# Kernel tuning notes

Hardware: AMD Instinct MI355X
Metric: run time of the kernel (lower is better)

## Reference

```python
import jax, jax.numpy as jnp
import numpy as np

N, T, H, O, S, R = 64, 1024, 256, 80, 128, 2


def _lin(k, fin, fout):
    kw, kb = jax.random.split(k)
    s = 1.0 / np.sqrt(fin)
    return (jax.random.uniform(kw, (fout, fin), jnp.float32, -s, s),
            jax.random.uniform(kb, (fout,), jnp.float32, -s, s))


def _gru_params(k, fin, hid):
    k1, k2, k3, k4 = jax.random.split(k, 4)
    s = 1.0 / np.sqrt(hid)
    u = lambda kk, shp: jax.random.uniform(kk, shp, jnp.float32, -s, s)
    return u(k1, (3 * hid, fin)), u(k2, (3 * hid, hid)), u(k3, (3 * hid,)), u(k4, (3 * hid,))


def setup_inputs() -> dict:
    key = jax.random.key(0)
    ks = jax.random.split(key, 16)
    inp = {}
    inp["input_enc"] = jax.random.normal(ks[0], (N, T, 2 * H), jnp.float32)
    inp["input_attW_enc"] = jax.random.normal(ks[1], (N, T, 2 * H), jnp.float32)
    inp["input_dec"] = jax.random.normal(ks[2], (N, O), jnp.float32)
    inp["style_vec"] = jax.random.normal(ks[3], (N, 1, S), jnp.float32)
    lengths = jnp.sort(jax.random.randint(ks[4], (N,), 1, T + 1))[::-1]
    inp["lengths_enc"] = lengths.at[0].set(T)  # pack_padded requires max(len)==T, descending
    inp["pw1"], inp["pb1"] = _lin(ks[5], O, 2 * H)
    inp["pw2"], inp["pb2"] = _lin(ks[6], 2 * H, H)
    inp["wdec"], inp["bdec"] = _lin(ks[7], 2 * H, 2 * H)
    inp["ga_ih"], inp["ga_hh"], inp["ga_bih"], inp["ga_bhh"] = _gru_params(ks[8], 3 * H + S, 2 * H)
    inp["wattn"], inp["battn"] = _lin(ks[9], 2 * H, 1)
    inp["wsc"], inp["bsc"] = _lin(ks[10], 4 * H + S, 2 * H)
    inp["g1_ih"], inp["g1_hh"], inp["g1_bih"], inp["g1_bhh"] = _gru_params(ks[11], 4 * H + S, 2 * H)
    inp["g2_ih"], inp["g2_hh"], inp["g2_bih"], inp["g2_bhh"] = _gru_params(ks[12], 2 * H, 2 * H)
    inp["wout"], inp["bout"] = _lin(ks[13], 2 * H, R * O)
    return inp


def _gru_cell(x, h, w_ih, w_hh, b_ih, b_hh):
    # PyTorch GRU cell: gates order (r, z, n)
    gi = x @ w_ih.T + b_ih
    gh = h @ w_hh.T + b_hh
    ir, iz, inn = jnp.split(gi, 3, -1)
    hr, hz, hn = jnp.split(gh, 3, -1)
    r = jax.nn.sigmoid(ir + hr)
    z = jax.nn.sigmoid(iz + hz)
    n = jnp.tanh(inn + r * hn)
    return (1.0 - z) * n + z * h


def reference(input_enc, input_attW_enc, input_dec, style_vec,
              pw1, pb1, pw2, pb2, wdec, bdec,
              ga_ih, ga_hh, ga_bih, ga_bhh,
              wattn, battn, wsc, bsc,
              g1_ih, g1_hh, g1_bih, g1_bhh,
              g2_ih, g2_hh, g2_bih, g2_bhh,
              wout, bout, lengths_enc):
    Nn, Tt, D2 = input_enc.shape
    Hh = D2 // 2
    # prenet (dropout disabled: eval-mode reference)
    pre = jax.nn.relu(jax.nn.relu(input_dec @ pw1.T + pb1) @ pw2.T + pb2)  # (N,H)
    ctx0 = jnp.zeros((Nn, 2 * Hh), input_enc.dtype)  # input_context=None -> zeros
    sv = style_vec[:, 0, :]
    x_att = jnp.concatenate([pre, ctx0, sv], axis=-1)  # (N,3H+S)
    h0 = jnp.zeros((Nn, 2 * Hh), input_enc.dtype)  # hidden states start None -> zeros
    out_att = _gru_cell(x_att, h0, ga_ih, ga_hh, ga_bih, ga_bhh)  # (N,2H)
    attW_dec = out_att @ wdec.T + bdec  # (N,2H), broadcast over T (expand_as)
    e = jnp.tanh(input_attW_enc + attW_dec[:, None, :])  # (N,T,2H)
    score = e @ wattn.T + battn  # (N,T,1)
    mask = (jnp.arange(Tt)[None, :] < lengths_enc[:, None]).astype(score.dtype)[..., None]
    w = jnp.exp(score) * mask  # pack/pad zeroes padded positions
    w = w / jnp.maximum(jnp.sum(w, axis=1, keepdims=True), 1e-12)  # F.normalize(p=1, dim=1)
    attn_applied = jnp.einsum('nt,ntd->nd', w[..., 0], input_enc)  # bmm(w^T, enc) -> (N,2H)
    out_dec = jnp.concatenate([attn_applied, out_att, sv], axis=-1)  # (N,4H+S)
    residual = out_dec @ wsc.T + bsc
    h1 = _gru_cell(out_dec, h0, g1_ih, g1_hh, g1_bih, g1_bhh)
    residual = residual + h1
    h2 = _gru_cell(residual, h0, g2_ih, g2_hh, g2_bih, g2_bhh)
    residual = residual + h2
    output = (residual @ wout.T + bout).reshape(Nn, R, -1)  # (N,r,O)
    return output, attn_applied[:, None, :]
```

## Files before the change

kernel.cpp:

```cpp
#include <hip/hip_runtime.h>
#include <math.h>

#define NB  64
#define TT  1024
#define H2  512
#define SS  128
#define OO  80
#define FIN_A 896
#define FIN_1 1152
#define CH  32

__device__ __forceinline__ float fast_rcp(float x) { return __builtin_amdgcn_rcpf(x); }
__device__ __forceinline__ float fast_sigmoid(float x) { return fast_rcp(1.0f + __expf(-x)); }
__device__ __forceinline__ float fast_tanh(float x) {
    float e = __expf(2.0f * x);
    return 1.0f - 2.0f * fast_rcp(e + 1.0f);
}
__device__ __forceinline__ float wred(float p) {
    #pragma unroll
    for (int o = 32; o > 0; o >>= 1) p += __shfl_xor(p, o, 64);
    return p;
}

__global__ void k_l1(const float* __restrict__ xdec, const float* __restrict__ pw1,
                     const float* __restrict__ pb1, const float* __restrict__ sv,
                     float* __restrict__ t1T, float* __restrict__ xaT,
                     float* __restrict__ out_decT) {
    int wv = threadIdx.x >> 6, lane = threadIdx.x & 63;
    if (blockIdx.x < 128) {
        int i = blockIdx.x * 4 + wv;
        const float* w = pw1 + i * OO;
        const float* x = xdec + lane * OO;
        float acc = 0.0f;
        #pragma unroll 8
        for (int k = 0; k < OO; ++k) acc += w[k] * x[k];
        t1T[i * 64 + lane] = fmaxf(acc + pb1[i], 0.0f);
    } else {
        int s = (blockIdx.x - 128) * 4 + wv;
        float v = sv[lane * SS + s];
        xaT[(256 + s) * 64 + lane] = v;
        out_decT[(1024 + s) * 64 + lane] = v;
    }
}

__global__ __launch_bounds__(512) void k_l2(const float* __restrict__ t1T,
                                            const float* __restrict__ pw2,
                                            const float* __restrict__ pb2,
                                            float* __restrict__ xaT) {
    int i = blockIdx.x;
    int wv = threadIdx.x >> 6, lane = threadIdx.x & 63;
    int k0 = wv * 64;
    const float* w = pw2 + (size_t)i * H2 + k0;
    const float* xT = t1T + k0 * 64;
    float p = 0.0f;
    #pragma unroll 8
    for (int k = 0; k < 64; ++k) p += w[k] * xT[k * 64 + lane];
    __shared__ float s[8][64];
    s[wv][lane] = p;
    __syncthreads();
    if (wv == 0) {
        float acc = 0.0f;
        #pragma unroll
        for (int q = 0; q < 8; ++q) acc += s[q][lane];
        xaT[i * 64 + lane] = fmaxf(acc + pb2[i], 0.0f);
    }
}

__global__ __launch_bounds__(512) void k_gruA(const float* __restrict__ xaT,
                                              const float* __restrict__ ga_ih,
                                              const float* __restrict__ ga_bih,
                                              const float* __restrict__ ga_bhh,
                                              float* __restrict__ out_decT) {
    int j = blockIdx.x;
    int wv = threadIdx.x >> 6, lane = threadIdx.x & 63;
    int k0 = wv * 48;
    const float* wr = ga_ih + (size_t)j * FIN_A;
    const float* wz = ga_ih + (size_t)(H2 + j) * FIN_A;
    const float* wn = ga_ih + (size_t)(2 * H2 + j) * FIN_A;
    float pr = 0.0f, pz = 0.0f, pn = 0.0f;
    #pragma unroll 8
    for (int kk = 0; kk < 48; ++kk) {
        int k = k0 + kk;
        int wc = k + (k >= 256 ? 512 : 0);
        float xv = xaT[k * 64 + lane];
        pr += wr[wc] * xv; pz += wz[wc] * xv; pn += wn[wc] * xv;
    }
    __shared__ float s[3][8][64];
    s[0][wv][lane] = pr; s[1][wv][lane] = pz; s[2][wv][lane] = pn;
    __syncthreads();
    if (wv == 0) {
        float fr = 0.0f, fz = 0.0f, fn = 0.0f;
        #pragma unroll
        for (int q = 0; q < 8; ++q) { fr += s[0][q][lane]; fz += s[1][q][lane]; fn += s[2][q][lane]; }
        float r = fast_sigmoid(fr + ga_bih[j] + ga_bhh[j]);
        float z = fast_sigmoid(fz + ga_bih[H2 + j] + ga_bhh[H2 + j]);
        float nn = fast_tanh(fn + ga_bih[2 * H2 + j] + r * ga_bhh[2 * H2 + j]);
        out_decT[(H2 + j) * 64 + lane] = (1.0f - z) * nn;
    }
}

__global__ __launch_bounds__(512) void k_attw(const float* __restrict__ out_decT,
                                              const float* __restrict__ wdec,
                                              const float* __restrict__ bdec,
                                              float* __restrict__ attW_dec) {
    int i = blockIdx.x;
    int wv = threadIdx.x >> 6, lane = threadIdx.x & 63;
    int k0 = wv * 64;
    const float* w = wdec + (size_t)i * H2 + k0;
    const float* xT = out_decT + (H2 + k0) * 64;
    float p = 0.0f;
    #pragma unroll 8
    for (int k = 0; k < 64; ++k) p += w[k] * xT[k * 64 + lane];
    __shared__ float s[8][64];
    s[wv][lane] = p;
    __syncthreads();
    if (wv == 0) {
        float acc = 0.0f;
        #pragma unroll
        for (int q = 0; q < 8; ++q) acc += s[q][lane];
        attW_dec[lane * H2 + i] = acc + bdec[i];
    }
}

__global__ __launch_bounds__(256) void k_attn(
        const float* __restrict__ enc, const float* __restrict__ attw_enc,
        const float* __restrict__ attW_dec, const float* __restrict__ wattn,
        const float* __restrict__ battn, const int* __restrict__ lengths,
        float* __restrict__ num_part ,
        float* __restrict__ den_part ) {
    int p = blockIdx.y;
    int c = blockIdx.x;
    int wv = threadIdx.x >> 6, lane = threadIdx.x & 63;
    int t0 = c * (TT / CH);
    __shared__ float sew[TT / CH];
    __shared__ float s[4 * 512];
    __shared__ float sd[4];
    const float4* w4 = (const float4*)wattn;
    float b = battn[0];

    #pragma unroll
    for (int half = 0; half < 2; ++half) {
        int n = half ? (63 - p) : p;
        int len = lengths[n];

        {
            const float4* d4 = (const float4*)(attW_dec + n * H2);
            #pragma unroll
            for (int r = 0; r < 8; ++r) {
                int t = t0 + wv * 8 + r;
                float val = 0.0f;
                if (t < len) {
                    const float4* e4 = (const float4*)(attw_enc + ((size_t)(n * TT + t)) * H2);
                    float pp = 0.0f;
                    #pragma unroll
                    for (int m = 0; m < 2; ++m) {
                        int idx = lane + m * 64;
                        float4 e = e4[idx], d = d4[idx], w = w4[idx];
                        pp += fast_tanh(e.x + d.x) * w.x + fast_tanh(e.y + d.y) * w.y +
                              fast_tanh(e.z + d.z) * w.z + fast_tanh(e.w + d.w) * w.w;
                    }
                    pp = wred(pp);
                    val = __expf(pp + b);
                }
                if (lane == 0) sew[wv * 8 + r] = val;
            }
        }
        __syncthreads();

        int d0 = lane * 8;
        const float* base = enc + ((size_t)(n * TT + t0 + wv * 8)) * H2 + d0;
        float4 a0 = {0, 0, 0, 0}, a1 = {0, 0, 0, 0};
        float dp = 0.0f;
        #pragma unroll
        for (int r = 0; r < 8; ++r) {
            float wt = sew[wv * 8 + r];
            if (wt != 0.0f) {
                const float4* v4 = (const float4*)(base + (size_t)r * H2);
                float4 v0 = v4[0], v1 = v4[1];
                a0.x += wt * v0.x; a0.y += wt * v0.y; a0.z += wt * v0.z; a0.w += wt * v0.w;
                a1.x += wt * v1.x; a1.y += wt * v1.y; a1.z += wt * v1.z; a1.w += wt * v1.w;
                dp += wt;
            }
        }
        float4* srow = (float4*)(s + wv * 512 + d0);
        srow[0] = a0; srow[1] = a1;
        if (lane == 0) sd[wv] = dp;
        __syncthreads();
        int d = threadIdx.x;
        float r0 = s[d] + s[512 + d] + s[1024 + d] + s[1536 + d];
        float r1 = s[256 + d] + s[768 + d] + s[1280 + d] + s[1792 + d];
        float* np = num_part + ((size_t)(c * NB + n)) * H2;
        np[d] = r0;
        np[256 + d] = r1;
        if (threadIdx.x == 0) den_part[c * NB + n] = sd[0] + sd[1] + sd[2] + sd[3];
        __syncthreads();
    }
}

__global__ void k_reduce(const float* __restrict__ num_part, const float* __restrict__ den_part,
                         float* __restrict__ out, float* __restrict__ out_decT) {
    int n = blockIdx.x;
    int d = blockIdx.y * 256 + threadIdx.x;
    float s = 0.0f, den = 0.0f;
    #pragma unroll 8
    for (int c = 0; c < CH; ++c) {
        s += num_part[((size_t)(c * NB + n)) * H2 + d];
        den += den_part[c * NB + n];
    }
    float a = s / fmaxf(den, 1e-12f);
    out[NB * 160 + n * H2 + d] = a;
    out_decT[(size_t)d * 64 + n] = a;
}

__global__ __launch_bounds__(512) void k_sc_h1(const float* __restrict__ out_decT,
                                               const float* __restrict__ wsc,
                                               const float* __restrict__ bsc,
                                               const float* __restrict__ g1_ih,
                                               const float* __restrict__ g1_bih,
                                               const float* __restrict__ g1_bhh,
                                               float* __restrict__ res1T) {
    int j = blockIdx.x;
    int wv = threadIdx.x >> 6, lane = threadIdx.x & 63;
    int k0 = wv * 144;
    const float* ws_ = wsc + (size_t)j * FIN_1 + k0;
    const float* wr = g1_ih + (size_t)j * FIN_1 + k0;
    const float* wz = g1_ih + (size_t)(H2 + j) * FIN_1 + k0;
    const float* wn = g1_ih + (size_t)(2 * H2 + j) * FIN_1 + k0;
    const float* xT = out_decT + k0 * 64;
    float2 ps = {0, 0}, pr = {0, 0}, pz = {0, 0}, pn = {0, 0};
    #pragma unroll 4
    for (int k = 0; k < 144; k += 2) {
        float x0 = xT[k * 64 + lane];
        float x1 = xT[(k + 1) * 64 + lane];
        float2 a = *(const float2*)(ws_ + k);
        float2 bb = *(const float2*)(wr + k);
        float2 cc = *(const float2*)(wz + k);
        float2 dd = *(const float2*)(wn + k);
        ps.x += a.x * x0; ps.y += a.y * x1;
        pr.x += bb.x * x0; pr.y += bb.y * x1;
        pz.x += cc.x * x0; pz.y += cc.y * x1;
        pn.x += dd.x * x0; pn.y += dd.y * x1;
    }
    __shared__ float s[4][8][64];
    s[0][wv][lane] = ps.x + ps.y; s[1][wv][lane] = pr.x + pr.y;
    s[2][wv][lane] = pz.x + pz.y; s[3][wv][lane] = pn.x + pn.y;
    __syncthreads();
    if (wv == 0) {
        float fs = 0.0f, fr = 0.0f, fz = 0.0f, fn = 0.0f;
        #pragma unroll
        for (int q = 0; q < 8; ++q) {
            fs += s[0][q][lane]; fr += s[1][q][lane];
            fz += s[2][q][lane]; fn += s[3][q][lane];
        }
        float r = fast_sigmoid(fr + g1_bih[j] + g1_bhh[j]);
        float z = fast_sigmoid(fz + g1_bih[H2 + j] + g1_bhh[H2 + j]);
        float nn = fast_tanh(fn + g1_bih[2 * H2 + j] + r * g1_bhh[2 * H2 + j]);
        res1T[j * 64 + lane] = fs + bsc[j] + (1.0f - z) * nn;
    }
}

__global__ __launch_bounds__(512) void k_h2(const float* __restrict__ res1T,
                                            const float* __restrict__ g2_ih,
                                            const float* __restrict__ g2_bih,
                                            const float* __restrict__ g2_bhh,
                                            float* __restrict__ res2T) {
    int j = blockIdx.x;
    int wv = threadIdx.x >> 6, lane = threadIdx.x & 63;
    int k0 = wv * 64;
    const float* wr = g2_ih + (size_t)j * H2 + k0;
    const float* wz = g2_ih + (size_t)(H2 + j) * H2 + k0;
    const float* wn = g2_ih + (size_t)(2 * H2 + j) * H2 + k0;
    const float* xT = res1T + k0 * 64;
    float pr = 0.0f, pz = 0.0f, pn = 0.0f;
    #pragma unroll 8
    for (int k = 0; k < 64; ++k) {
        float xv = xT[k * 64 + lane];
        pr += wr[k] * xv; pz += wz[k] * xv; pn += wn[k] * xv;
    }
    __shared__ float s[3][8][64];
    s[0][wv][lane] = pr; s[1][wv][lane] = pz; s[2][wv][lane] = pn;
    __syncthreads();
    if (wv == 0) {
        float fr = 0.0f, fz = 0.0f, fn = 0.0f;
        #pragma unroll
        for (int q = 0; q < 8; ++q) { fr += s[0][q][lane]; fz += s[1][q][lane]; fn += s[2][q][lane]; }
        float r = fast_sigmoid(fr + g2_bih[j] + g2_bhh[j]);
        float z = fast_sigmoid(fz + g2_bih[H2 + j] + g2_bhh[H2 + j]);
        float nn = fast_tanh(fn + g2_bih[2 * H2 + j] + r * g2_bhh[2 * H2 + j]);
        res2T[j * 64 + lane] = res1T[j * 64 + lane] + (1.0f - z) * nn;
    }
}

__global__ __launch_bounds__(512) void k_out(const float* __restrict__ res2T,
                                             const float* __restrict__ wout,
                                             const float* __restrict__ bout,
                                             float* __restrict__ out) {
    int i = blockIdx.x;
    int wv = threadIdx.x >> 6, lane = threadIdx.x & 63;
    int k0 = wv * 64;
    const float* w = wout + (size_t)i * H2 + k0;
    const float* xT = res2T + k0 * 64;
    float p = 0.0f;
    #pragma unroll 8
    for (int k = 0; k < 64; ++k) p += w[k] * xT[k * 64 + lane];
    __shared__ float s[8][64];
    s[wv][lane] = p;
    __syncthreads();
    if (wv == 0) {
        float acc = 0.0f;
        #pragma unroll
        for (int q = 0; q < 8; ++q) acc += s[q][lane];
        out[lane * 160 + i] = acc + bout[i];
    }
}

extern "C" void kernel_launch(void* const* d_in, const int* in_sizes, int n_in,
                              void* d_out, int out_size, void* d_ws, size_t ws_size,
                              hipStream_t stream) {
    const float* input_enc      = (const float*)d_in[0];
    const float* input_attW_enc = (const float*)d_in[1];
    const float* input_dec      = (const float*)d_in[2];
    const float* style_vec      = (const float*)d_in[3];
    const int*   lengths_enc    = (const int*)d_in[4];
    const float* pw1  = (const float*)d_in[5];
    const float* pb1  = (const float*)d_in[6];
    const float* pw2  = (const float*)d_in[7];
    const float* pb2  = (const float*)d_in[8];
    const float* wdec = (const float*)d_in[9];
    const float* bdec = (const float*)d_in[10];
    const float* ga_ih  = (const float*)d_in[11];
    const float* ga_bih = (const float*)d_in[13];
    const float* ga_bhh = (const float*)d_in[14];
    const float* wattn  = (const float*)d_in[15];
    const float* battn  = (const float*)d_in[16];
    const float* wsc    = (const float*)d_in[17];
    const float* bsc    = (const float*)d_in[18];
    const float* g1_ih  = (const float*)d_in[19];
    const float* g1_bih = (const float*)d_in[21];
    const float* g1_bhh = (const float*)d_in[22];
    const float* g2_ih  = (const float*)d_in[23];
    const float* g2_bih = (const float*)d_in[25];
    const float* g2_bhh = (const float*)d_in[26];
    const float* wout   = (const float*)d_in[27];
    const float* bout   = (const float*)d_in[28];
    float* out = (float*)d_out;

    float* ws = (float*)d_ws;
    float* num_part = ws;
    float* den_part = ws + 1048576;
    float* t1T      = ws + 1050624;
    float* xaT      = ws + 1083392;
    float* out_decT = ws + 1107968;
    float* attW_dec = ws + 1181696;
    float* res1T    = ws + 1214464;
    float* res2T    = ws + 1247232;

    k_l1<<<160, 256, 0, stream>>>(input_dec, pw1, pb1, style_vec, t1T, xaT, out_decT);
    k_l2<<<256, 512, 0, stream>>>(t1T, pw2, pb2, xaT);
    k_gruA<<<512, 512, 0, stream>>>(xaT, ga_ih, ga_bih, ga_bhh, out_decT);
    k_attw<<<512, 512, 0, stream>>>(out_decT, wdec, bdec, attW_dec);
    k_attn<<<dim3(CH, 32), 256, 0, stream>>>(input_enc, input_attW_enc, attW_dec,
                                             wattn, battn, lengths_enc, num_part, den_part);
    k_reduce<<<dim3(64, 2), 256, 0, stream>>>(num_part, den_part, out, out_decT);
    k_sc_h1<<<512, 512, 0, stream>>>(out_decT, wsc, bsc, g1_ih, g1_bih, g1_bhh, res1T);
    k_h2<<<512, 512, 0, stream>>>(res1T, g2_ih, g2_bih, g2_bhh, res2T);
    k_out<<<160, 512, 0, stream>>>(res2T, wout, bout, out);
}
```

Measured before the change: 383.3 us.

## Fuse all stages into one cooperative persistent kernel with grid syncs

Replaces the nine separate kernel launches with a single cooperative kernel of 1024 blocks that runs every stage in sequence, separated by grid-wide barriers. Stages keep the prior per-block work mapping, with 256-thread blocks replacing the earlier 512-thread ones for the GEMV stages. The aim is to remove launch gaps and per-kernel tail effects. In exchange it adds eight grid.sync barriers and leaves many blocks idle in the small stages. It falls back to the old multi-kernel path if cooperative launch or the required occupancy is unavailable.

```diff
diff --git a/kernel.cpp b/kernel.cpp
--- a/kernel.cpp
+++ b/kernel.cpp
@@ -1,5 +1,8 @@
 #include <hip/hip_runtime.h>
+#include <hip/hip_cooperative_groups.h>
 #include <math.h>
+
+namespace cg = cooperative_groups;
 
 #define NB  64
 #define TT  1024
@@ -20,6 +23,289 @@
     #pragma unroll
     for (int o = 32; o > 0; o >>= 1) p += __shfl_xor(p, o, 64);
     return p;
+}
+
+__global__ __launch_bounds__(256, 4) void mega(
+        const float* __restrict__ enc, const float* __restrict__ attw_enc,
+        const float* __restrict__ xdec, const float* __restrict__ sv,
+        const int* __restrict__ lengths,
+        const float* __restrict__ pw1, const float* __restrict__ pb1,
+        const float* __restrict__ pw2, const float* __restrict__ pb2,
+        const float* __restrict__ wdec, const float* __restrict__ bdec,
+        const float* __restrict__ ga_ih, const float* __restrict__ ga_bih,
+        const float* __restrict__ ga_bhh,
+        const float* __restrict__ wattn, const float* __restrict__ battn,
+        const float* __restrict__ wsc, const float* __restrict__ bsc,
+        const float* __restrict__ g1_ih, const float* __restrict__ g1_bih,
+        const float* __restrict__ g1_bhh,
+        const float* __restrict__ g2_ih, const float* __restrict__ g2_bih,
+        const float* __restrict__ g2_bhh,
+        const float* __restrict__ wout, const float* __restrict__ bout,
+        float* __restrict__ out,
+        float* __restrict__ num_part, float* __restrict__ den_part,
+        float* __restrict__ t1T, float* __restrict__ xaT,
+        float* __restrict__ out_decT, float* __restrict__ attW_dec,
+        float* __restrict__ res1T, float* __restrict__ res2T) {
+    cg::grid_group grid = cg::this_grid();
+    int b = blockIdx.x;
+    int wv = threadIdx.x >> 6, lane = threadIdx.x & 63;
+    __shared__ float smem[2112];
+
+    if (b < 128) {
+        int i = b * 4 + wv;
+        const float* w = pw1 + i * OO;
+        const float* x = xdec + lane * OO;
+        float acc = 0.0f;
+        #pragma unroll 8
+        for (int k = 0; k < OO; ++k) acc += w[k] * x[k];
+        t1T[i * 64 + lane] = fmaxf(acc + pb1[i], 0.0f);
+    } else if (b < 160) {
+        int s = (b - 128) * 4 + wv;
+        float v = sv[lane * SS + s];
+        xaT[(256 + s) * 64 + lane] = v;
+        out_decT[(1024 + s) * 64 + lane] = v;
+    }
+    grid.sync();
+
+    if (b < 256) {
+        int i = b, k0 = wv * 128;
+        const float* w = pw2 + (size_t)i * H2 + k0;
+        const float* xT = t1T + k0 * 64;
+        float p = 0.0f;
+        #pragma unroll 8
+        for (int k = 0; k < 128; ++k) p += w[k] * xT[k * 64 + lane];
+        smem[wv * 64 + lane] = p;
+        __syncthreads();
+        if (wv == 0) {
+            float acc = smem[lane] + smem[64 + lane] + smem[128 + lane] + smem[192 + lane];
+            xaT[i * 64 + lane] = fmaxf(acc + pb2[i], 0.0f);
+        }
+    }
+    grid.sync();
+
+    if (b < 512) {
+        int j = b, k0 = wv * 96;
+        const float* wr = ga_ih + (size_t)j * FIN_A;
+        const float* wz = ga_ih + (size_t)(H2 + j) * FIN_A;
+        const float* wn = ga_ih + (size_t)(2 * H2 + j) * FIN_A;
+        float pr = 0.0f, pz = 0.0f, pn = 0.0f;
+        #pragma unroll 8
+        for (int kk = 0; kk < 96; ++kk) {
+            int k = k0 + kk;
+            int wc = k + (k >= 256 ? 512 : 0);
+            float xv = xaT[k * 64 + lane];
+            pr += wr[wc] * xv; pz += wz[wc] * xv; pn += wn[wc] * xv;
+        }
+        smem[wv * 64 + lane] = pr;
+        smem[256 + wv * 64 + lane] = pz;
+        smem[512 + wv * 64 + lane] = pn;
+        __syncthreads();
+        if (wv == 0) {
+            float fr = 0.0f, fz = 0.0f, fn = 0.0f;
+            #pragma unroll
+            for (int q = 0; q < 4; ++q) {
+                fr += smem[q * 64 + lane];
+                fz += smem[256 + q * 64 + lane];
+                fn += smem[512 + q * 64 + lane];
+            }
+            float r = fast_sigmoid(fr + ga_bih[j] + ga_bhh[j]);
+            float z = fast_sigmoid(fz + ga_bih[H2 + j] + ga_bhh[H2 + j]);
+            float nn = fast_tanh(fn + ga_bih[2 * H2 + j] + r * ga_bhh[2 * H2 + j]);
+            out_decT[(H2 + j) * 64 + lane] = (1.0f - z) * nn;
+        }
+    }
+    grid.sync();
+
+    if (b < 512) {
+        int i = b, k0 = wv * 128;
+        const float* w = wdec + (size_t)i * H2 + k0;
+        const float* xT = out_decT + (H2 + k0) * 64;
+        float p = 0.0f;
+        #pragma unroll 8
+        for (int k = 0; k < 128; ++k) p += w[k] * xT[k * 64 + lane];
+        __syncthreads();
+        smem[wv * 64 + lane] = p;
+        __syncthreads();
+        if (wv == 0) {
+            float acc = smem[lane] + smem[64 + lane] + smem[128 + lane] + smem[192 + lane];
+            attW_dec[lane * H2 + i] = acc + bdec[i];
+        }
+    }
+    grid.sync();
+
+    {
+        int c = b & 31, p = b >> 5;
+        int t0 = c * (TT / CH);
+        float* sew = smem;
+        float* sd = smem + 32;
+        float* s = smem + 64;
+        const float4* w4 = (const float4*)wattn;
+        float bb = battn[0];
+        #pragma unroll
+        for (int half = 0; half < 2; ++half) {
+            int n = half ? (63 - p) : p;
+            int len = lengths[n];
+            {
+                const float4* d4 = (const float4*)(attW_dec + n * H2);
+                #pragma unroll
+                for (int r = 0; r < 8; ++r) {
+                    int t = t0 + wv * 8 + r;
+                    float val = 0.0f;
+                    if (t < len) {
+                        const float4* e4 = (const float4*)(attw_enc + ((size_t)(n * TT + t)) * H2);
+                        float pp = 0.0f;
+                        #pragma unroll
+                        for (int m = 0; m < 2; ++m) {
+                            int idx = lane + m * 64;
+                            float4 e = e4[idx], d = d4[idx], w = w4[idx];
+                            pp += fast_tanh(e.x + d.x) * w.x + fast_tanh(e.y + d.y) * w.y +
+                                  fast_tanh(e.z + d.z) * w.z + fast_tanh(e.w + d.w) * w.w;
+                        }
+                        pp = wred(pp);
+                        val = __expf(pp + bb);
+                    }
+                    if (lane == 0) sew[wv * 8 + r] = val;
+                }
+            }
+            __syncthreads();
+            int d0 = lane * 8;
+            const float* base = enc + ((size_t)(n * TT + t0 + wv * 8)) * H2 + d0;
+            float4 a0 = {0, 0, 0, 0}, a1 = {0, 0, 0, 0};
+            float dp = 0.0f;
+            #pragma unroll
+            for (int r = 0; r < 8; ++r) {
+                float wt = sew[wv * 8 + r];
+                if (wt != 0.0f) {
+                    const float4* v4 = (const float4*)(base + (size_t)r * H2);
+                    float4 v0 = v4[0], v1 = v4[1];
+                    a0.x += wt * v0.x; a0.y += wt * v0.y; a0.z += wt * v0.z; a0.w += wt * v0.w;
+                    a1.x += wt * v1.x; a1.y += wt * v1.y; a1.z += wt * v1.z; a1.w += wt * v1.w;
+                    dp += wt;
+                }
+            }
+            float4* srow = (float4*)(s + wv * 512 + d0);
+            srow[0] = a0; srow[1] = a1;
+            if (lane == 0) sd[wv] = dp;
+            __syncthreads();
+            int d = threadIdx.x;
+            float r0 = s[d] + s[512 + d] + s[1024 + d] + s[1536 + d];
+            float r1 = s[256 + d] + s[768 + d] + s[1280 + d] + s[1792 + d];
+            float* np = num_part + ((size_t)(c * NB + n)) * H2;
+            np[d] = r0;
+            np[256 + d] = r1;
+            if (threadIdx.x == 0) den_part[c * NB + n] = sd[0] + sd[1] + sd[2] + sd[3];
+            __syncthreads();
+        }
+    }
+    grid.sync();
+
+    if (b < 128) {
+        int n = b >> 1;
+        int d = (b & 1) * 256 + threadIdx.x;
+        float s = 0.0f, den = 0.0f;
+        #pragma unroll 8
+        for (int c = 0; c < CH; ++c) {
+            s += num_part[((size_t)(c * NB + n)) * H2 + d];
+            den += den_part[c * NB + n];
+        }
+        float a = s / fmaxf(den, 1e-12f);
+        out[NB * 160 + n * H2 + d] = a;
+        out_decT[(size_t)d * 64 + n] = a;
+    }
+    grid.sync();
+
+    if (b < 512) {
+        int j = b, k0 = wv * 288;
+        const float* ws_ = wsc + (size_t)j * FIN_1 + k0;
+        const float* wr = g1_ih + (size_t)j * FIN_1 + k0;
+        const float* wz = g1_ih + (size_t)(H2 + j) * FIN_1 + k0;
+        const float* wn = g1_ih + (size_t)(2 * H2 + j) * FIN_1 + k0;
+        const float* xT = out_decT + k0 * 64;
+        float2 ps = {0, 0}, pr = {0, 0}, pz = {0, 0}, pn = {0, 0};
+        #pragma unroll 4
+        for (int k = 0; k < 288; k += 2) {
+            float x0 = xT[k * 64 + lane];
+            float x1 = xT[(k + 1) * 64 + lane];
+            float2 a = *(const float2*)(ws_ + k);
+            float2 bb2 = *(const float2*)(wr + k);
+            float2 cc = *(const float2*)(wz + k);
+            float2 dd = *(const float2*)(wn + k);
+            ps.x += a.x * x0; ps.y += a.y * x1;
+            pr.x += bb2.x * x0; pr.y += bb2.y * x1;
+            pz.x += cc.x * x0; pz.y += cc.y * x1;
+            pn.x += dd.x * x0; pn.y += dd.y * x1;
+        }
+        __syncthreads();
+        smem[wv * 64 + lane] = ps.x + ps.y;
+        smem[256 + wv * 64 + lane] = pr.x + pr.y;
+        smem[512 + wv * 64 + lane] = pz.x + pz.y;
+        smem[768 + wv * 64 + lane] = pn.x + pn.y;
+        __syncthreads();
+        if (wv == 0) {
+            float fs = 0.0f, fr = 0.0f, fz = 0.0f, fn = 0.0f;
+            #pragma unroll
+            for (int q = 0; q < 4; ++q) {
+                fs += smem[q * 64 + lane];
+                fr += smem[256 + q * 64 + lane];
+                fz += smem[512 + q * 64 + lane];
+                fn += smem[768 + q * 64 + lane];
+            }
+            float r = fast_sigmoid(fr + g1_bih[j] + g1_bhh[j]);
+            float z = fast_sigmoid(fz + g1_bih[H2 + j] + g1_bhh[H2 + j]);
+            float nn = fast_tanh(fn + g1_bih[2 * H2 + j] + r * g1_bhh[2 * H2 + j]);
+            res1T[j * 64 + lane] = fs + bsc[j] + (1.0f - z) * nn;
+        }
+    }
+    grid.sync();
+
+    if (b < 512) {
+        int j = b, k0 = wv * 128;
+        const float* wr = g2_ih + (size_t)j * H2 + k0;
+        const float* wz = g2_ih + (size_t)(H2 + j) * H2 + k0;
+        const float* wn = g2_ih + (size_t)(2 * H2 + j) * H2 + k0;
+        const float* xT = res1T + k0 * 64;
+        float pr = 0.0f, pz = 0.0f, pn = 0.0f;
+        #pragma unroll 8
+        for (int k = 0; k < 128; ++k) {
+            float xv = xT[k * 64 + lane];
+            pr += wr[k] * xv; pz += wz[k] * xv; pn += wn[k] * xv;
+        }
+        __syncthreads();
+        smem[wv * 64 + lane] = pr;
+        smem[256 + wv * 64 + lane] = pz;
+        smem[512 + wv * 64 + lane] = pn;
+        __syncthreads();
+        if (wv == 0) {
+            float fr = 0.0f, fz = 0.0f, fn = 0.0f;
+            #pragma unroll
+            for (int q = 0; q < 4; ++q) {
+                fr += smem[q * 64 + lane];
+                fz += smem[256 + q * 64 + lane];
+                fn += smem[512 + q * 64 + lane];
+            }
+            float r = fast_sigmoid(fr + g2_bih[j] + g2_bhh[j]);
+            float z = fast_sigmoid(fz + g2_bih[H2 + j] + g2_bhh[H2 + j]);
+            float nn = fast_tanh(fn + g2_bih[2 * H2 + j] + r * g2_bhh[2 * H2 + j]);
+            res2T[j * 64 + lane] = res1T[j * 64 + lane] + (1.0f - z) * nn;
+        }
+    }
+    grid.sync();
+
+    if (b < 160) {
+        int i = b, k0 = wv * 128;
+        const float* w = wout + (size_t)i * H2 + k0;
+        const float* xT = res2T + k0 * 64;
+        float p = 0.0f;
+        #pragma unroll 8
+        for (int k = 0; k < 128; ++k) p += w[k] * xT[k * 64 + lane];
+        __syncthreads();
+        smem[wv * 64 + lane] = p;
+        __syncthreads();
+        if (wv == 0) {
+            float acc = smem[lane] + smem[64 + lane] + smem[128 + lane] + smem[192 + lane];
+            out[lane * 160 + i] = acc + bout[i];
+        }
+    }
 }
 
 __global__ void k_l1(const float* __restrict__ xdec, const float* __restrict__ pw1,
@@ -126,8 +412,7 @@
         const float* __restrict__ enc, const float* __restrict__ attw_enc,
         const float* __restrict__ attW_dec, const float* __restrict__ wattn,
         const float* __restrict__ battn, const int* __restrict__ lengths,
-        float* __restrict__ num_part ,
-        float* __restrict__ den_part ) {
+        float* __restrict__ num_part, float* __restrict__ den_part) {
     int p = blockIdx.y;
     int c = blockIdx.x;
     int wv = threadIdx.x >> 6, lane = threadIdx.x & 63;
@@ -142,7 +427,6 @@
     for (int half = 0; half < 2; ++half) {
         int n = half ? (63 - p) : p;
         int len = lengths[n];
-
         {
             const float4* d4 = (const float4*)(attW_dec + n * H2);
             #pragma unroll
@@ -166,7 +450,6 @@
             }
         }
         __syncthreads();
-
         int d0 = lane * 8;
         const float* base = enc + ((size_t)(n * TT + t0 + wv * 8)) * H2 + d0;
         float4 a0 = {0, 0, 0, 0}, a1 = {0, 0, 0, 0};
@@ -355,14 +638,42 @@
     float* res1T    = ws + 1214464;
     float* res2T    = ws + 1247232;
 
-    k_l1<<<160, 256, 0, stream>>>(input_dec, pw1, pb1, style_vec, t1T, xaT, out_decT);
-    k_l2<<<256, 512, 0, stream>>>(t1T, pw2, pb2, xaT);
-    k_gruA<<<512, 512, 0, stream>>>(xaT, ga_ih, ga_bih, ga_bhh, out_decT);
-    k_attw<<<512, 512, 0, stream>>>(out_decT, wdec, bdec, attW_dec);
-    k_attn<<<dim3(CH, 32), 256, 0, stream>>>(input_enc, input_attW_enc, attW_dec,
-                                             wattn, battn, lengths_enc, num_part, den_part);
-    k_reduce<<<dim3(64, 2), 256, 0, stream>>>(num_part, den_part, out, out_decT);
-    k_sc_h1<<<512, 512, 0, stream>>>(out_decT, wsc, bsc, g1_ih, g1_bih, g1_bhh, res1T);
-    k_h2<<<512, 512, 0, stream>>>(res1T, g2_ih, g2_bih, g2_bhh, res2T);
-    k_out<<<160, 512, 0, stream>>>(res2T, wout, bout, out);
-}
+    bool coop_ok = false;
+    int maxBlocksPerCU = 0;
+    if (hipOccupancyMaxActiveBlocksPerMultiprocessor(&maxBlocksPerCU, (const void*)mega,
+                                                     256, 0) == hipSuccess &&
+        maxBlocksPerCU >= 4) {
+        void* args[] = {
+            (void*)&input_enc, (void*)&input_attW_enc, (void*)&input_dec, (void*)&style_vec,
+            (void*)&lengths_enc,
+            (void*)&pw1, (void*)&pb1, (void*)&pw2, (void*)&pb2,
+            (void*)&wdec, (void*)&bdec,
+            (void*)&ga_ih, (void*)&ga_bih, (void*)&ga_bhh,
+            (void*)&wattn, (void*)&battn,
+            (void*)&wsc, (void*)&bsc,
+            (void*)&g1_ih, (void*)&g1_bih, (void*)&g1_bhh,
+            (void*)&g2_ih, (void*)&g2_bih, (void*)&g2_bhh,
+            (void*)&wout, (void*)&bout,
+            (void*)&out,
+            (void*)&num_part, (void*)&den_part, (void*)&t1T, (void*)&xaT,
+            (void*)&out_decT, (void*)&attW_dec, (void*)&res1T, (void*)&res2T
+        };
+        if (hipLaunchCooperativeKernel((const void*)mega, dim3(1024), dim3(256),
+                                       args, 0, stream) == hipSuccess) {
+            coop_ok = true;
+        }
+    }
+
+    if (!coop_ok) {
+        k_l1<<<160, 256, 0, stream>>>(input_dec, pw1, pb1, style_vec, t1T, xaT, out_decT);
+        k_l2<<<256, 512, 0, stream>>>(t1T, pw2, pb2, xaT);
+        k_gruA<<<512, 512, 0, stream>>>(xaT, ga_ih, ga_bih, ga_bhh, out_decT);
+        k_attw<<<512, 512, 0, stream>>>(out_decT, wdec, bdec, attW_dec);
+        k_attn<<<dim3(CH, 32), 256, 0, stream>>>(input_enc, input_attW_enc, attW_dec,
+                                                 wattn, battn, lengths_enc, num_part, den_part);
+        k_reduce<<<dim3(64, 2), 256, 0, stream>>>(num_part, den_part, out, out_decT);
+        k_sc_h1<<<512, 512, 0, stream>>>(out_decT, wsc, bsc, g1_ih, g1_bih, g1_bhh, res1T);
+        k_h2<<<512, 512, 0, stream>>>(res1T, g2_ih, g2_bih, g2_bhh, res2T);
+        k_out<<<160, 512, 0, stream>>>(res2T, wout, bout, out);
+    }
+}
```

Result: no change. 390.0 us (+1.7%).

## Fuse decoder prenet, attention GRU and attW projection into one per-batch kernel

Applied to the files above, without the earlier changes.

Replaces four kernels (prenet layer 1, layer 2, attention GRU, decoder attention projection) with a single kernel that runs one 1024-thread block per batch row and keeps intermediates in shared memory. This removes three launches, their global-memory round trips and the gaps between kernels. In exchange, each of the 64 blocks re-reads all the weight matrices (about 7 MB in total), so weight traffic goes up 64-fold, mostly served from L2. Only 64 blocks run, so most of the GPU's CUs sit idle.

```diff
diff --git a/kernel.cpp b/kernel.cpp
--- a/kernel.cpp
+++ b/kernel.cpp
@@ -22,103 +22,89 @@
     return p;
 }
 
-__global__ void k_l1(const float* __restrict__ xdec, const float* __restrict__ pw1,
-                     const float* __restrict__ pb1, const float* __restrict__ sv,
-                     float* __restrict__ t1T, float* __restrict__ xaT,
-                     float* __restrict__ out_decT) {
-    int wv = threadIdx.x >> 6, lane = threadIdx.x & 63;
-    if (blockIdx.x < 128) {
-        int i = blockIdx.x * 4 + wv;
+__global__ __launch_bounds__(1024) void k_dec(
+        const float* __restrict__ xdec, const float* __restrict__ sv,
+        const float* __restrict__ pw1, const float* __restrict__ pb1,
+        const float* __restrict__ pw2, const float* __restrict__ pb2,
+        const float* __restrict__ ga_ih, const float* __restrict__ ga_bih,
+        const float* __restrict__ ga_bhh,
+        const float* __restrict__ wdec, const float* __restrict__ bdec,
+        float* __restrict__ out_decT, float* __restrict__ attW_dec) {
+    int n = blockIdx.x;
+    int wv = threadIdx.x >> 6, lane = threadIdx.x & 63;
+    __shared__ float st1[512];
+    __shared__ float spre[256];
+    __shared__ float ssv[128];
+    __shared__ float satt[512];
+
+    if (threadIdx.x < 128) {
+        float v = sv[n * SS + threadIdx.x];
+        ssv[threadIdx.x] = v;
+        out_decT[(1024 + threadIdx.x) * 64 + n] = v;
+    }
+
+    const float* x0 = xdec + n * OO;
+    float xa = (lane < OO) ? x0[lane] : 0.0f;
+    float xb = (lane < OO - 64) ? x0[64 + lane] : 0.0f;
+    for (int o = 0; o < 32; ++o) {
+        int i = wv * 32 + o;
         const float* w = pw1 + i * OO;
-        const float* x = xdec + lane * OO;
-        float acc = 0.0f;
-        #pragma unroll 8
-        for (int k = 0; k < OO; ++k) acc += w[k] * x[k];
-        t1T[i * 64 + lane] = fmaxf(acc + pb1[i], 0.0f);
-    } else {
-        int s = (blockIdx.x - 128) * 4 + wv;
-        float v = sv[lane * SS + s];
-        xaT[(256 + s) * 64 + lane] = v;
-        out_decT[(1024 + s) * 64 + lane] = v;
-    }
-}
-
-__global__ __launch_bounds__(512) void k_l2(const float* __restrict__ t1T,
-                                            const float* __restrict__ pw2,
-                                            const float* __restrict__ pb2,
-                                            float* __restrict__ xaT) {
-    int i = blockIdx.x;
-    int wv = threadIdx.x >> 6, lane = threadIdx.x & 63;
-    int k0 = wv * 64;
-    const float* w = pw2 + (size_t)i * H2 + k0;
-    const float* xT = t1T + k0 * 64;
-    float p = 0.0f;
-    #pragma unroll 8
-    for (int k = 0; k < 64; ++k) p += w[k] * xT[k * 64 + lane];
-    __shared__ float s[8][64];
-    s[wv][lane] = p;
-    __syncthreads();
-    if (wv == 0) {
-        float acc = 0.0f;
-        #pragma unroll
-        for (int q = 0; q < 8; ++q) acc += s[q][lane];
-        xaT[i * 64 + lane] = fmaxf(acc + pb2[i], 0.0f);
-    }
-}
-
-__global__ __launch_bounds__(512) void k_gruA(const float* __restrict__ xaT,
-                                              const float* __restrict__ ga_ih,
-                                              const float* __restrict__ ga_bih,
-                                              const float* __restrict__ ga_bhh,
-                                              float* __restrict__ out_decT) {
-    int j = blockIdx.x;
-    int wv = threadIdx.x >> 6, lane = threadIdx.x & 63;
-    int k0 = wv * 48;
-    const float* wr = ga_ih + (size_t)j * FIN_A;
-    const float* wz = ga_ih + (size_t)(H2 + j) * FIN_A;
-    const float* wn = ga_ih + (size_t)(2 * H2 + j) * FIN_A;
-    float pr = 0.0f, pz = 0.0f, pn = 0.0f;
-    #pragma unroll 8
-    for (int kk = 0; kk < 48; ++kk) {
-        int k = k0 + kk;
-        int wc = k + (k >= 256 ? 512 : 0);
-        float xv = xaT[k * 64 + lane];
-        pr += wr[wc] * xv; pz += wz[wc] * xv; pn += wn[wc] * xv;
-    }
-    __shared__ float s[3][8][64];
-    s[0][wv][lane] = pr; s[1][wv][lane] = pz; s[2][wv][lane] = pn;
-    __syncthreads();
-    if (wv == 0) {
-        float fr = 0.0f, fz = 0.0f, fn = 0.0f;
-        #pragma unroll
-        for (int q = 0; q < 8; ++q) { fr += s[0][q][lane]; fz += s[1][q][lane]; fn += s[2][q][lane]; }
-        float r = fast_sigmoid(fr + ga_bih[j] + ga_bhh[j]);
-        float z = fast_sigmoid(fz + ga_bih[H2 + j] + ga_bhh[H2 + j]);
-        float nn = fast_tanh(fn + ga_bih[2 * H2 + j] + r * ga_bhh[2 * H2 + j]);
-        out_decT[(H2 + j) * 64 + lane] = (1.0f - z) * nn;
-    }
-}
-
-__global__ __launch_bounds__(512) void k_attw(const float* __restrict__ out_decT,
-                                              const float* __restrict__ wdec,
-                                              const float* __restrict__ bdec,
-                                              float* __restrict__ attW_dec) {
-    int i = blockIdx.x;
-    int wv = threadIdx.x >> 6, lane = threadIdx.x & 63;
-    int k0 = wv * 64;
-    const float* w = wdec + (size_t)i * H2 + k0;
-    const float* xT = out_decT + (H2 + k0) * 64;
-    float p = 0.0f;
-    #pragma unroll 8
-    for (int k = 0; k < 64; ++k) p += w[k] * xT[k * 64 + lane];
-    __shared__ float s[8][64];
-    s[wv][lane] = p;
-    __syncthreads();
-    if (wv == 0) {
-        float acc = 0.0f;
-        #pragma unroll
-        for (int q = 0; q < 8; ++q) acc += s[q][lane];
-        attW_dec[lane * H2 + i] = acc + bdec[i];
+        float wa = (lane < OO) ? w[lane] : 0.0f;
+        float wb = (lane < OO - 64) ? w[64 + lane] : 0.0f;
+        float p = wred(xa * wa + xb * wb);
+        if (lane == 0) st1[i] = fmaxf(p + pb1[i], 0.0f);
+    }
+    __syncthreads();
+
+    for (int o = 0; o < 16; ++o) {
+        int i = wv * 16 + o;
+        const float* w = pw2 + (size_t)i * H2;
+        float p = 0.0f;
+        #pragma unroll
+        for (int m = 0; m < 8; ++m) { int k = lane + 64 * m; p += w[k] * st1[k]; }
+        p = wred(p);
+        if (lane == 0) spre[i] = fmaxf(p + pb2[i], 0.0f);
+    }
+    __syncthreads();
+
+    for (int o = 0; o < 32; ++o) {
+        int j = wv * 32 + o;
+        const float* wr = ga_ih + (size_t)j * FIN_A;
+        const float* wz = ga_ih + (size_t)(H2 + j) * FIN_A;
+        const float* wn = ga_ih + (size_t)(2 * H2 + j) * FIN_A;
+        float pr = 0.0f, pz = 0.0f, pn = 0.0f;
+        #pragma unroll
+        for (int m = 0; m < 4; ++m) {
+            int k = lane + 64 * m;
+            float xv = spre[k];
+            pr += wr[k] * xv; pz += wz[k] * xv; pn += wn[k] * xv;
+        }
+        #pragma unroll
+        for (int m = 0; m < 2; ++m) {
+            int k = lane + 64 * m;
+            float xv = ssv[k];
+            pr += wr[768 + k] * xv; pz += wz[768 + k] * xv; pn += wn[768 + k] * xv;
+        }
+        pr = wred(pr); pz = wred(pz); pn = wred(pn);
+        if (lane == 0) {
+            float r = fast_sigmoid(pr + ga_bih[j] + ga_bhh[j]);
+            float z = fast_sigmoid(pz + ga_bih[H2 + j] + ga_bhh[H2 + j]);
+            float nn = fast_tanh(pn + ga_bih[2 * H2 + j] + r * ga_bhh[2 * H2 + j]);
+            float oa = (1.0f - z) * nn;
+            satt[j] = oa;
+            out_decT[(H2 + j) * 64 + n] = oa;
+        }
+    }
+    __syncthreads();
+
+    for (int o = 0; o < 32; ++o) {
+        int i = wv * 32 + o;
+        const float* w = wdec + (size_t)i * H2;
+        float p = 0.0f;
+        #pragma unroll
+        for (int m = 0; m < 8; ++m) { int k = lane + 64 * m; p += w[k] * satt[k]; }
+        p = wred(p);
+        if (lane == 0) attW_dec[n * H2 + i] = p + bdec[i];
     }
 }
 
@@ -142,7 +128,6 @@
     for (int half = 0; half < 2; ++half) {
         int n = half ? (63 - p) : p;
         int len = lengths[n];
-
         {
             const float4* d4 = (const float4*)(attW_dec + n * H2);
             #pragma unroll
@@ -166,7 +151,6 @@
             }
         }
         __syncthreads();
-
         int d0 = lane * 8;
         const float* base = enc + ((size_t)(n * TT + t0 + wv * 8)) * H2 + d0;
         float4 a0 = {0, 0, 0, 0}, a1 = {0, 0, 0, 0};
@@ -348,17 +332,14 @@
     float* ws = (float*)d_ws;
     float* num_part = ws;
     float* den_part = ws + 1048576;
-    float* t1T      = ws + 1050624;
-    float* xaT      = ws + 1083392;
-    float* out_decT = ws + 1107968;
-    float* attW_dec = ws + 1181696;
-    float* res1T    = ws + 1214464;
-    float* res2T    = ws + 1247232;
-
-    k_l1<<<160, 256, 0, stream>>>(input_dec, pw1, pb1, style_vec, t1T, xaT, out_decT);
-    k_l2<<<256, 512, 0, stream>>>(t1T, pw2, pb2, xaT);
-    k_gruA<<<512, 512, 0, stream>>>(xaT, ga_ih, ga_bih, ga_bhh, out_decT);
-    k_attw<<<512, 512, 0, stream>>>(out_decT, wdec, bdec, attW_dec);
+    float* out_decT = ws + 1050624;
+    float* attW_dec = ws + 1124352;
+    float* res1T    = ws + 1157120;
+    float* res2T    = ws + 1189888;
+
+    k_dec<<<64, 1024, 0, stream>>>(input_dec, style_vec, pw1, pb1, pw2, pb2,
+                                   ga_ih, ga_bih, ga_bhh, wdec, bdec,
+                                   out_decT, attW_dec);
     k_attn<<<dim3(CH, 32), 256, 0, stream>>>(input_enc, input_attW_enc, attW_dec,
                                              wattn, battn, lengths_enc, num_part, den_part);
     k_reduce<<<dim3(64, 2), 256, 0, stream>>>(num_part, den_part, out, out_decT);
```

Result: slower. 474.1 us (+23.7%).
